# Optimization experiments

Measured on AMD Instinct MI355X. Metric: run time of the kernel, lower is better.

## Reference

```python
import jax, jax.numpy as jnp
import numpy as np

B, T_IN, N, C_IN = 4, 16, 5000, 16
HID, C_OUT, KSZ, K_CHEB = 32, 64, 3, 3
E = 80000
BN_EPS = 1e-5


def _conv1xk(x, W, b):
    # x: (B,C,N,T), W: (O,I,1,k) -> (B,O,N,T-k+1)
    y = jax.lax.conv_general_dilated(x, W, (1, 1), 'VALID',
                                     dimension_numbers=('NCHW', 'OIHW', 'NCHW'))
    return y + b[None, :, None, None]


def temporal_conv(X, W1, b1, W2, b2, W3, b3):
    # X: (B,T,N,C) -> (B,T-k+1,N,O); gated temporal conv (GLU-style)
    Xp = jnp.transpose(X, (0, 3, 2, 1))  # (B,C,N,T)
    P = _conv1xk(Xp, W1, b1)
    Q = jax.nn.sigmoid(_conv1xk(Xp, W2, b2))
    R = _conv1xk(Xp, W3, b3)
    H = jax.nn.relu(P * Q + R)
    return jnp.transpose(H, (0, 3, 2, 1))


def cheb_conv(x, edge_index, edge_weight, W, b, lambda_max=2.0):
    # x: (B,T,N,C). Batched ChebConv with sym normalization (PyG semantics).
    n = x.shape[2]
    row, col = edge_index[0], edge_index[1]
    deg = jax.ops.segment_sum(edge_weight, row, num_segments=n)
    dis = jnp.where(deg > 0, deg ** -0.5, 0.0)
    w_norm = dis[row] * edge_weight * dis[col]  # (E,)

    def lhat(z):
        # A_norm z via scatter-add over edges, batched over (B,T)
        az = jnp.zeros_like(z).at[:, :, row, :].add(
            w_norm[None, None, :, None] * z[:, :, col, :])
        # L z = z - A_norm z ; L_hat = (2/lmax) L - I
        return (2.0 / lambda_max) * (z - az) - z

    Tx0 = x
    out = jnp.einsum('btnc,cd->btnd', Tx0, W[0])
    Tx1 = lhat(Tx0)
    out = out + jnp.einsum('btnc,cd->btnd', Tx1, W[1])
    for k in range(2, W.shape[0]):
        Tx2 = 2.0 * lhat(Tx1) - Tx0
        out = out + jnp.einsum('btnc,cd->btnd', Tx2, W[k])
        Tx0, Tx1 = Tx1, Tx2
    return out + b


def batch_norm_nodes(T, gamma, beta):
    # torch: permute to (B, N, T, C), BatchNorm2d(num_nodes), permute back
    Tp = jnp.transpose(T, (0, 2, 1, 3))  # (B,N,T,C)
    mean = jnp.mean(Tp, axis=(0, 2, 3), keepdims=True)
    var = jnp.mean((Tp - mean) ** 2, axis=(0, 2, 3), keepdims=True)  # biased
    Tn = (Tp - mean) / jnp.sqrt(var + BN_EPS)
    Tn = Tn * gamma[None, :, None, None] + beta[None, :, None, None]
    return jnp.transpose(Tn, (0, 2, 1, 3))


def setup_inputs() -> dict:
    key = jax.random.key(0)
    ks = jax.random.split(key, 20)
    s = 0.05
    inp = {
        'X': jax.random.normal(ks[0], (B, T_IN, N, C_IN), jnp.float32),
        'edge_index': jax.random.randint(ks[1], (2, E), 0, N, jnp.int64
                                         if jax.config.jax_enable_x64 else jnp.int32),
        'edge_weight': jax.random.uniform(ks[2], (E,), jnp.float32),
        'tc1_w1': jax.random.normal(ks[3], (HID, C_IN, 1, KSZ)) * s,
        'tc1_b1': jnp.zeros((HID,)),
        'tc1_w2': jax.random.normal(ks[4], (HID, C_IN, 1, KSZ)) * s,
        'tc1_b2': jnp.zeros((HID,)),
        'tc1_w3': jax.random.normal(ks[5], (HID, C_IN, 1, KSZ)) * s,
        'tc1_b3': jnp.zeros((HID,)),
        'cheb_W': jax.random.normal(ks[6], (K_CHEB, HID, HID)) * s,
        'cheb_b': jnp.zeros((HID,)),
        'tc2_w1': jax.random.normal(ks[7], (C_OUT, HID, 1, KSZ)) * s,
        'tc2_b1': jnp.zeros((C_OUT,)),
        'tc2_w2': jax.random.normal(ks[8], (C_OUT, HID, 1, KSZ)) * s,
        'tc2_b2': jnp.zeros((C_OUT,)),
        'tc2_w3': jax.random.normal(ks[9], (C_OUT, HID, 1, KSZ)) * s,
        'tc2_b3': jnp.zeros((C_OUT,)),
        'bn_gamma': jnp.ones((N,)),
        'bn_beta': jnp.zeros((N,)),
    }
    return inp


def reference(X, edge_index, edge_weight,
              tc1_w1, tc1_b1, tc1_w2, tc1_b2, tc1_w3, tc1_b3,
              cheb_W, cheb_b,
              tc2_w1, tc2_b1, tc2_w2, tc2_b2, tc2_w3, tc2_b3,
              bn_gamma, bn_beta):
    T0 = temporal_conv(X, tc1_w1, tc1_b1, tc1_w2, tc1_b2, tc1_w3, tc1_b3)
    T = jax.nn.relu(cheb_conv(T0, edge_index, edge_weight, cheb_W, cheb_b))
    T = temporal_conv(T, tc2_w1, tc2_b1, tc2_w2, tc2_b2, tc2_w3, tc2_b3)
    return batch_norm_nodes(T, bn_gamma, bn_beta)
```

## Files before the change

### kernel.cpp

```cpp
#include <hip/hip_runtime.h>
#include <hip/hip_bf16.h>

#define STC_N     5000
#define STC_TIN   16
#define STC_T1    14
#define STC_T2    12
#define STC_CIN   16
#define STC_CH    32
#define STC_CO    64
#define STC_BT1   56
#define STC_BT2   48
#define STC_RT1   17500
#define STC_GBLK  1280
#define STC_GWAVE (STC_GBLK*4)
#define STC_ROWB1 1792

#define STC_OFF_DEG   0
#define STC_OFF_CNT   20000
#define STC_OFF_CUR   40000
#define STC_OFF_DIS   60000
#define STC_OFF_OFFS  80000
#define STC_OFF_WN    100032
#define STC_OFF_CCOL  420032
#define STC_OFF_CW    740032
#define STC_OFF_T0    1060096
#define STC_OFF_G1    (STC_OFF_T0 + 17920000)
#define STC_OFF_G2    (STC_OFF_G1 + 17920000)
#define STC_OFF_PK2   (STC_OFF_G2 + 17920000)
#define STC_OFF_PK1   (STC_OFF_PK2 + 36864)
#define STC_OFF_PKC   (STC_OFF_PK1 + 12288)
#define STC_WS_REQ    (STC_OFF_PKC + 6144)

typedef __hip_bfloat16 bf16;
typedef short stc_s8 __attribute__((ext_vector_type(8)));
typedef float stc_f4 __attribute__((ext_vector_type(4)));

__device__ float stc_lo16(unsigned u) { return __uint_as_float(u << 16); }
__device__ float stc_hi16(unsigned u) { return __uint_as_float(u & 0xffff0000u); }
__device__ float stc_s2f(short s) {
    return __uint_as_float(((unsigned)(unsigned short)s) << 16);
}

__device__ short stc_f2bs(float f) {
    unsigned u = __float_as_uint(f);
    u = (u + 0x7FFFu + ((u >> 16) & 1u)) >> 16;
    return (short)u;
}

__global__ void STConv_9972914061616_kernel() {}

__global__ void stc_fill(float* out, int n, float val) {
    int i = blockIdx.x * 256 + threadIdx.x;
    if (i < n) out[i] = val;
}

__global__ void stc_init(int* zp,
                         const float* w1a, const float* w1b, const float* w1c,
                         const float* w2a, const float* w2b, const float* w2c,
                         const float* chW,
                         short* pk1, short* pk2, short* pkc) {
    if (blockIdx.x < 59) {
        int i = blockIdx.x * 256 + threadIdx.x;
        if (i < 15000) zp[i] = 0;
        return;
    }
    int gid = (blockIdx.x - 59) * 256 + threadIdx.x;
    if (gid >= 54 * 64) return;
    int fi = gid >> 6;
    int lane = gid & 63;
    int j = lane & 15;
    int quad = lane >> 4;
    short f[8];
    if (fi < 36) {
        int s = fi % 3;
        int cc4 = fi / 3;
        int conv = cc4 >> 2;
        int c4 = cc4 & 3;
        const float* Wp = (conv == 0) ? w2a : ((conv == 1) ? w2b : w2c);
        int och = c4 * 16 + j;
        for (int i = 0; i < 8; ++i) {
            int cc = quad * 8 + i;
            f[i] = stc_f2bs(Wp[och * 96 + cc * 3 + s]);
        }
        for (int i = 0; i < 8; ++i) pk2[(fi * 64 + lane) * 8 + i] = f[i];
    } else if (fi < 48) {
        int t = fi - 36;
        int s = t & 1;
        int cj = t >> 1;
        int conv = cj >> 1;
        int jt = cj & 1;
        const float* Wp = (conv == 0) ? w1a : ((conv == 1) ? w1b : w1c);
        int och = jt * 16 + j;
        for (int i = 0; i < 8; ++i) {
            int k = s * 32 + quad * 8 + i;
            int kt = k >> 4;
            int c = k & 15;
            f[i] = (kt < 3) ? stc_f2bs(Wp[och * 48 + c * 3 + kt]) : (short)0;
        }
        for (int i = 0; i < 8; ++i) pk1[(t * 64 + lane) * 8 + i] = f[i];
    } else {
        int t = fi - 48;
        int s = t >> 1;
        int jt = t & 1;
        int d = jt * 16 + j;
        for (int i = 0; i < 8; ++i) {
            int c = quad * 8 + i;
            float w0 = chW[c * 32 + d];
            float w1 = chW[1024 + c * 32 + d];
            float w2 = chW[2048 + c * 32 + d];
            float v = (s == 0) ? (w0 - w2) : ((s == 1) ? -w1 : 2.0f * w2);
            f[i] = stc_f2bs(v);
        }
        for (int i = 0; i < 8; ++i) pkc[(t * 64 + lane) * 8 + i] = f[i];
    }
}

__global__ void stc_deg(const int* ei, const float* ew, float* deg, int E) {
    int e = blockIdx.x * 256 + threadIdx.x;
    if (e < E) atomicAdd(&deg[ei[e]], ew[e]);
}

__global__ void stc_wnorm(const int* ei, const float* ew, const float* deg,
                          float* wn, int* cnt, int E) {
    int e = blockIdx.x * 256 + threadIdx.x;
    if (e < E) {
        int r = ei[e];
        int c = ei[E + e];
        float dr = deg[r];
        float dc = deg[c];
        float ir = (dr > 0.0f) ? rsqrtf(dr) : 0.0f;
        float ic = (dc > 0.0f) ? rsqrtf(dc) : 0.0f;
        wn[e] = ir * ew[e] * ic;
        atomicAdd(&cnt[r], 1);
    }
}

__global__ void stc_scan(const int* cnt, int* offs, int n) {
    __shared__ int s[256];
    int tid = threadIdx.x;
    int base = tid * 20;
    int loc[20];
    int sum = 0;
#pragma unroll
    for (int k = 0; k < 20; ++k) {
        int i = base + k;
        int v = (i < n) ? cnt[i] : 0;
        loc[k] = sum;
        sum += v;
    }
    s[tid] = sum;
    __syncthreads();
    for (int off = 1; off < 256; off <<= 1) {
        int t = (tid >= off) ? s[tid - off] : 0;
        __syncthreads();
        s[tid] += t;
        __syncthreads();
    }
    int pre = (tid > 0) ? s[tid - 1] : 0;
#pragma unroll
    for (int k = 0; k < 20; ++k) {
        int i = base + k;
        if (i < n) offs[i] = pre + loc[k];
    }
    if (tid == 255) offs[n] = s[255];
}

__global__ void stc_scatter(const int* ei, const float* wn, const int* offs,
                            int* cursor, int* ccol, float* cw, int E) {
    int e = blockIdx.x * 256 + threadIdx.x;
    if (e < E) {
        int r = ei[e];
        int pos = atomicAdd(&cursor[r], 1);
        int slot = offs[r] + pos;
        ccol[slot] = ei[E + e];
        cw[slot] = wn[e];
    }
}

__global__ __launch_bounds__(256, 2) void stc_tconv1m(
    const float* X, const short* pk1,
    const float* B1, const float* B2, const float* B3,
    bf16* T0) {
    int lane = threadIdx.x & 63;
    int j = lane & 15;
    int quad = lane >> 4;
    int wave = blockIdx.x * 4 + (threadIdx.x >> 6);

    stc_s8 bfrag[3][2][2];
    for (int conv = 0; conv < 3; ++conv)
        for (int jt = 0; jt < 2; ++jt)
            for (int s = 0; s < 2; ++s) {
                int t = (conv * 2 + jt) * 2 + s;
                bfrag[conv][jt][s] = *(const stc_s8*)(pk1 + (t * 64 + lane) * 8);
            }
    float pb[2], qb[2], rb[2];
    for (int jt = 0; jt < 2; ++jt) {
        int och = jt * 16 + j;
        pb[jt] = B1[och];
        qb[jt] = B2[och];
        rb[jt] = B3[och];
    }

    for (int rt = wave; rt < STC_RT1; rt += STC_GWAVE) {
        int rm = rt * 16 + j;
        int n = rm % STC_N;
        int bt = rm / STC_N;
        int t = bt % STC_T1;
        int b = bt / STC_T1;

        int kt0 = quad >> 1;
        int c0 = (quad & 1) * 8;
        const float* xp0 = X + ((size_t)((b * STC_TIN + t + kt0) * STC_N + n)) * STC_CIN + c0;
        stc_s8 af0;
        for (int i = 0; i < 8; ++i) af0[i] = stc_f2bs(xp0[i]);

        stc_s8 af1;
        if (quad < 2) {
            const float* xp1 = X + ((size_t)((b * STC_TIN + t + 2) * STC_N + n)) * STC_CIN + c0;
            for (int i = 0; i < 8; ++i) af1[i] = stc_f2bs(xp1[i]);
        } else {
            for (int i = 0; i < 8; ++i) af1[i] = 0;
        }

        stc_f4 acc[6];
        for (int a = 0; a < 6; ++a) acc[a] = (stc_f4){0.0f, 0.0f, 0.0f, 0.0f};
        for (int conv = 0; conv < 3; ++conv) {
            for (int jt = 0; jt < 2; ++jt) {
                int a = conv * 2 + jt;
                acc[a] = __builtin_amdgcn_mfma_f32_16x16x32_bf16(
                    af0, bfrag[conv][jt][0], acc[a], 0, 0, 0);
                acc[a] = __builtin_amdgcn_mfma_f32_16x16x32_bf16(
                    af1, bfrag[conv][jt][1], acc[a], 0, 0, 0);
            }
        }

        for (int jt = 0; jt < 2; ++jt) {
            for (int reg = 0; reg < 4; ++reg) {
                float P = acc[jt][reg] + pb[jt];
                float Q = acc[2 + jt][reg] + qb[jt];
                float R = acc[4 + jt][reg] + rb[jt];
                float Qc = fminf(fmaxf(Q, -30.0f), 30.0f);
                float sg = 1.0f / (1.0f + __expf(-Qc));
                float h = P * sg + R;
                if (h < 0.0f) h = 0.0f;
                int row = rt * 16 + quad * 4 + reg;
                int nw = row % STC_N;
                int btw = row / STC_N;
                T0[(size_t)nw * STC_ROWB1 + btw * STC_CH + jt * 16 + j] =
                    __float2bfloat16(h);
            }
        }
    }
}

__global__ void stc_gatherv(const bf16* z, bf16* g, const int* offs,
                            const int* ccol, const float* cw) {
    int n = blockIdx.x;
    __shared__ int col_s[128];
    __shared__ float w_s[128];
    int beg = offs[n];
    int end = offs[n + 1];
    int cg = threadIdx.x & 3;
    int sl = threadIdx.x >> 2;
    int act = (sl < STC_BT1);
    float a0 = 0.f, a1 = 0.f, a2 = 0.f, a3 = 0.f;
    float a4 = 0.f, a5 = 0.f, a6 = 0.f, a7 = 0.f;
    const bf16* zb = z + sl * STC_CH + cg * 8;
    for (int chunk = beg; chunk < end; chunk += 128) {
        int m = end - chunk;
        if (m > 128) m = 128;
        if (threadIdx.x < m) {
            col_s[threadIdx.x] = ccol[chunk + threadIdx.x];
            w_s[threadIdx.x] = cw[chunk + threadIdx.x];
        }
        __syncthreads();
        if (act) {
            int i = 0;
            for (; i + 4 <= m; i += 4) {
                float w0 = w_s[i], w1 = w_s[i + 1], w2 = w_s[i + 2], w3 = w_s[i + 3];
                uint4 u0 = *(const uint4*)(zb + (size_t)col_s[i] * STC_ROWB1);
                uint4 u1 = *(const uint4*)(zb + (size_t)col_s[i + 1] * STC_ROWB1);
                uint4 u2 = *(const uint4*)(zb + (size_t)col_s[i + 2] * STC_ROWB1);
                uint4 u3 = *(const uint4*)(zb + (size_t)col_s[i + 3] * STC_ROWB1);
                a0 += w0 * stc_lo16(u0.x); a1 += w0 * stc_hi16(u0.x);
                a2 += w0 * stc_lo16(u0.y); a3 += w0 * stc_hi16(u0.y);
                a4 += w0 * stc_lo16(u0.z); a5 += w0 * stc_hi16(u0.z);
                a6 += w0 * stc_lo16(u0.w); a7 += w0 * stc_hi16(u0.w);
                a0 += w1 * stc_lo16(u1.x); a1 += w1 * stc_hi16(u1.x);
                a2 += w1 * stc_lo16(u1.y); a3 += w1 * stc_hi16(u1.y);
                a4 += w1 * stc_lo16(u1.z); a5 += w1 * stc_hi16(u1.z);
                a6 += w1 * stc_lo16(u1.w); a7 += w1 * stc_hi16(u1.w);
                a0 += w2 * stc_lo16(u2.x); a1 += w2 * stc_hi16(u2.x);
                a2 += w2 * stc_lo16(u2.y); a3 += w2 * stc_hi16(u2.y);
                a4 += w2 * stc_lo16(u2.z); a5 += w2 * stc_hi16(u2.z);
                a6 += w2 * stc_lo16(u2.w); a7 += w2 * stc_hi16(u2.w);
                a0 += w3 * stc_lo16(u3.x); a1 += w3 * stc_hi16(u3.x);
                a2 += w3 * stc_lo16(u3.y); a3 += w3 * stc_hi16(u3.y);
                a4 += w3 * stc_lo16(u3.z); a5 += w3 * stc_hi16(u3.z);
                a6 += w3 * stc_lo16(u3.w); a7 += w3 * stc_hi16(u3.w);
            }
            for (; i < m; ++i) {
                float w = w_s[i];
                uint4 u = *(const uint4*)(zb + (size_t)col_s[i] * STC_ROWB1);
                a0 += w * stc_lo16(u.x); a1 += w * stc_hi16(u.x);
                a2 += w * stc_lo16(u.y); a3 += w * stc_hi16(u.y);
                a4 += w * stc_lo16(u.z); a5 += w * stc_hi16(u.z);
                a6 += w * stc_lo16(u.w); a7 += w * stc_hi16(u.w);
            }
        }
        __syncthreads();
    }
    if (act) {
        unsigned p0 = ((unsigned)(unsigned short)stc_f2bs(a0)) |
                      (((unsigned)(unsigned short)stc_f2bs(a1)) << 16);
        unsigned p1 = ((unsigned)(unsigned short)stc_f2bs(a2)) |
                      (((unsigned)(unsigned short)stc_f2bs(a3)) << 16);
        unsigned p2 = ((unsigned)(unsigned short)stc_f2bs(a4)) |
                      (((unsigned)(unsigned short)stc_f2bs(a5)) << 16);
        unsigned p3 = ((unsigned)(unsigned short)stc_f2bs(a6)) |
                      (((unsigned)(unsigned short)stc_f2bs(a7)) << 16);
        uint4 o;
        o.x = p0; o.y = p1; o.z = p2; o.w = p3;
        *(uint4*)(g + (size_t)n * STC_ROWB1 + sl * STC_CH + cg * 8) = o;
    }
}

__global__ __launch_bounds__(256, 2) void stc_combconv2bn(
    const bf16* T0, const bf16* G1, const bf16* G2,
    const short* pkc, const float* chB,
    const short* pk2, const float* B1, const float* B2, const float* B3,
    const float* gamma, const float* beta, float* T2) {
    __shared__ short comb[64 * 40];
    __shared__ short hb[48 * 72];
    __shared__ float red[8];
    int lane = threadIdx.x & 63;
    int j = lane & 15;
    int quad = lane >> 4;
    int w = threadIdx.x >> 6;
    int n = blockIdx.x;

    {
        stc_s8 cfrag[3][2];
        for (int s = 0; s < 3; ++s)
            for (int jt = 0; jt < 2; ++jt)
                cfrag[s][jt] = *(const stc_s8*)(pkc + ((s * 2 + jt) * 64 + lane) * 8);
        float bl0 = chB[j];
        float bl1 = chB[16 + j];
        size_t rm = (size_t)n * STC_BT1 + w * 16 + j;
        size_t abase = rm * STC_CH + quad * 8;
        stc_s8 a0 = *(const stc_s8*)(T0 + abase);
        stc_s8 a1 = *(const stc_s8*)(G1 + abase);
        stc_s8 a2 = *(const stc_s8*)(G2 + abase);
        stc_f4 acc[2];
        acc[0] = (stc_f4){0.0f, 0.0f, 0.0f, 0.0f};
        acc[1] = (stc_f4){0.0f, 0.0f, 0.0f, 0.0f};
        for (int jt = 0; jt < 2; ++jt) {
            acc[jt] = __builtin_amdgcn_mfma_f32_16x16x32_bf16(a0, cfrag[0][jt], acc[jt], 0, 0, 0);
            acc[jt] = __builtin_amdgcn_mfma_f32_16x16x32_bf16(a1, cfrag[1][jt], acc[jt], 0, 0, 0);
            acc[jt] = __builtin_amdgcn_mfma_f32_16x16x32_bf16(a2, cfrag[2][jt], acc[jt], 0, 0, 0);
        }
        for (int jt = 0; jt < 2; ++jt) {
            float bl = (jt == 0) ? bl0 : bl1;
            for (int reg = 0; reg < 4; ++reg) {
                float h = acc[jt][reg] + bl;
                if (h < 0.0f) h = 0.0f;
                int row = w * 16 + quad * 4 + reg;
                comb[row * 40 + jt * 16 + j] = stc_f2bs(h);
            }
        }
    }
    __syncthreads();

    stc_s8 bfrag[3][3];
    for (int conv = 0; conv < 3; ++conv)
        for (int s = 0; s < 3; ++s) {
            int fi = (conv * 4 + w) * 3 + s;
            bfrag[conv][s] = *(const stc_s8*)(pk2 + (fi * 64 + lane) * 8);
        }
    int och = w * 16 + j;
    float pb = B1[och];
    float qb = B2[och];
    float rb = B3[och];

    float lsum = 0.0f;
    for (int t3 = 0; t3 < 3; ++t3) {
        int btb = t3 * 16;
        int bt2 = btb + j;
        int b = bt2 / STC_T2;
        int t = bt2 % STC_T2;
        const short* ap = comb + (b * STC_T1 + t) * 40 + quad * 8;
        stc_s8 af0 = *(const stc_s8*)(ap);
        stc_s8 af1 = *(const stc_s8*)(ap + 40);
        stc_s8 af2 = *(const stc_s8*)(ap + 80);

        stc_f4 acc[3];
        for (int a = 0; a < 3; ++a) acc[a] = (stc_f4){0.0f, 0.0f, 0.0f, 0.0f};
        for (int conv = 0; conv < 3; ++conv) {
            acc[conv] = __builtin_amdgcn_mfma_f32_16x16x32_bf16(
                af0, bfrag[conv][0], acc[conv], 0, 0, 0);
            acc[conv] = __builtin_amdgcn_mfma_f32_16x16x32_bf16(
                af1, bfrag[conv][1], acc[conv], 0, 0, 0);
            acc[conv] = __builtin_amdgcn_mfma_f32_16x16x32_bf16(
                af2, bfrag[conv][2], acc[conv], 0, 0, 0);
        }

        for (int reg = 0; reg < 4; ++reg) {
            float P = acc[0][reg] + pb;
            float Q = acc[1][reg] + qb;
            float R = acc[2][reg] + rb;
            float Qc = fminf(fmaxf(Q, -30.0f), 30.0f);
            float sg = 1.0f / (1.0f + __expf(-Qc));
            float h = P * sg + R;
            if (h < 0.0f) h = 0.0f;
            short hs = stc_f2bs(h);
            int row = btb + quad * 4 + reg;
            hb[row * 72 + w * 16 + j] = hs;
            lsum += stc_s2f(hs);
        }
    }
    for (int off = 32; off; off >>= 1) lsum += __shfl_xor(lsum, off);
    if (lane == 0) red[w] = lsum;
    __syncthreads();

    float mean = (red[0] + red[1] + red[2] + red[3]) * (1.0f / (STC_BT2 * STC_CO));

    int colc = threadIdx.x & 63;
    int rw0 = threadIdx.x >> 6;
    float sq = 0.0f;
    for (int it = 0; it < 12; ++it) {
        int row = it * 4 + rw0;
        float d = stc_s2f(hb[row * 72 + colc]) - mean;
        sq += d * d;
    }
    for (int off = 32; off; off >>= 1) sq += __shfl_xor(sq, off);
    if (lane == 0) red[4 + w] = sq;
    __syncthreads();
    float var = (red[4] + red[5] + red[6] + red[7]) * (1.0f / (STC_BT2 * STC_CO));
    float istd = rsqrtf(var + 1e-5f);
    float scale = istd * gamma[n];
    float shift = beta[n] - mean * scale;
    for (int it = 0; it < 12; ++it) {
        int row = it * 4 + rw0;
        T2[((size_t)row * STC_N + n) * STC_CO + colc] =
            stc_s2f(hb[row * 72 + colc]) * scale + shift;
    }
}

extern "C" void kernel_launch(void* const* d_in, const int* in_sizes, int n_in,
                              void* d_out, int out_size, void* d_ws, size_t ws_size,
                              hipStream_t stream) {
    float* out = (float*)d_out;
    int outb = (out_size + 255) / 256;

    if (n_in < 19) {
        stc_fill<<<outb, 256, 0, stream>>>(out, out_size, 60.0f);
        return;
    }
    if (ws_size < (size_t)STC_WS_REQ) {
        stc_fill<<<outb, 256, 0, stream>>>(out, out_size, 50.0f);
        return;
    }

    const float* X = (const float*)d_in[0];
    const int* ei = (const int*)d_in[1];
    const float* ew = (const float*)d_in[2];
    const float* w1a = (const float*)d_in[3];
    const float* b1a = (const float*)d_in[4];
    const float* w1b = (const float*)d_in[5];
    const float* b1b = (const float*)d_in[6];
    const float* w1c = (const float*)d_in[7];
    const float* b1c = (const float*)d_in[8];
    const float* chW = (const float*)d_in[9];
    const float* chB = (const float*)d_in[10];
    const float* w2a = (const float*)d_in[11];
    const float* b2a = (const float*)d_in[12];
    const float* w2b = (const float*)d_in[13];
    const float* b2b = (const float*)d_in[14];
    const float* w2c = (const float*)d_in[15];
    const float* b2c = (const float*)d_in[16];
    const float* gam = (const float*)d_in[17];
    const float* bet = (const float*)d_in[18];
    int E = in_sizes[1] / 2;

    char* ws = (char*)d_ws;
    float* deg = (float*)(ws + STC_OFF_DEG);
    int* cnt = (int*)(ws + STC_OFF_CNT);
    int* cursor = (int*)(ws + STC_OFF_CUR);
    int* offs = (int*)(ws + STC_OFF_OFFS);
    float* wn = (float*)(ws + STC_OFF_WN);
    int* ccol = (int*)(ws + STC_OFF_CCOL);
    float* cw = (float*)(ws + STC_OFF_CW);
    bf16* T0 = (bf16*)(ws + STC_OFF_T0);
    bf16* G1 = (bf16*)(ws + STC_OFF_G1);
    bf16* G2 = (bf16*)(ws + STC_OFF_G2);
    short* pk2 = (short*)(ws + STC_OFF_PK2);
    short* pk1 = (short*)(ws + STC_OFF_PK1);
    short* pkc = (short*)(ws + STC_OFF_PKC);

    stc_init<<<73, 256, 0, stream>>>((int*)(ws + STC_OFF_DEG),
                                     w1a, w1b, w1c, w2a, w2b, w2c, chW,
                                     pk1, pk2, pkc);
    stc_deg<<<(E + 255) / 256, 256, 0, stream>>>(ei, ew, deg, E);
    stc_wnorm<<<(E + 255) / 256, 256, 0, stream>>>(ei, ew, deg, wn, cnt, E);
    stc_scan<<<1, 256, 0, stream>>>(cnt, offs, STC_N);
    stc_scatter<<<(E + 255) / 256, 256, 0, stream>>>(ei, wn, offs, cursor, ccol, cw, E);
    stc_tconv1m<<<STC_GBLK, 256, 0, stream>>>(X, pk1, b1a, b1b, b1c, T0);
    stc_gatherv<<<STC_N, 256, 0, stream>>>(T0, G1, offs, ccol, cw);
    stc_gatherv<<<STC_N, 256, 0, stream>>>(G1, G2, offs, ccol, cw);
    stc_combconv2bn<<<STC_N, 256, 0, stream>>>(
        T0, G1, G2, pkc, chB, pk2, b2a, b2b, b2c, gam, bet, out);
}
```

Measured before the change: 257.0 us.

## Fuse second graph gather into combine/conv2/BN kernel and merge edge-norm kernels

```diff
diff --git a/kernel.cpp b/kernel.cpp
--- a/kernel.cpp
+++ b/kernel.cpp
@@ -115,22 +115,11 @@
     }
 }
 
-__global__ void stc_deg(const int* ei, const float* ew, float* deg, int E) {
-    int e = blockIdx.x * 256 + threadIdx.x;
-    if (e < E) atomicAdd(&deg[ei[e]], ew[e]);
-}
-
-__global__ void stc_wnorm(const int* ei, const float* ew, const float* deg,
-                          float* wn, int* cnt, int E) {
+__global__ void stc_deg(const int* ei, const float* ew, float* deg, int* cnt, int E) {
     int e = blockIdx.x * 256 + threadIdx.x;
     if (e < E) {
         int r = ei[e];
-        int c = ei[E + e];
-        float dr = deg[r];
-        float dc = deg[c];
-        float ir = (dr > 0.0f) ? rsqrtf(dr) : 0.0f;
-        float ic = (dc > 0.0f) ? rsqrtf(dc) : 0.0f;
-        wn[e] = ir * ew[e] * ic;
+        atomicAdd(&deg[r], ew[e]);
         atomicAdd(&cnt[r], 1);
     }
 }
@@ -165,15 +154,21 @@
     if (tid == 255) offs[n] = s[255];
 }
 
-__global__ void stc_scatter(const int* ei, const float* wn, const int* offs,
-                            int* cursor, int* ccol, float* cw, int E) {
+__global__ void stc_scatter(const int* ei, const float* ew, const float* deg,
+                            const int* offs, int* cursor, int* ccol, float* cw,
+                            int E) {
     int e = blockIdx.x * 256 + threadIdx.x;
     if (e < E) {
         int r = ei[e];
+        int c = ei[E + e];
+        float dr = deg[r];
+        float dc = deg[c];
+        float ir = (dr > 0.0f) ? rsqrtf(dr) : 0.0f;
+        float ic = (dc > 0.0f) ? rsqrtf(dc) : 0.0f;
         int pos = atomicAdd(&cursor[r], 1);
         int slot = offs[r] + pos;
-        ccol[slot] = ei[E + e];
-        cw[slot] = wn[e];
+        ccol[slot] = c;
+        cw[slot] = ir * ew[e] * ic;
     }
 }
 
@@ -325,19 +320,91 @@
     }
 }
 
-__global__ __launch_bounds__(256, 2) void stc_combconv2bn(
-    const bf16* T0, const bf16* G1, const bf16* G2,
+__global__ __launch_bounds__(256, 2) void stc_gcombconv2bn(
+    const bf16* T0, const bf16* G1,
+    const int* offs, const int* ccol, const float* cw,
     const short* pkc, const float* chB,
     const short* pk2, const float* B1, const float* B2, const float* B3,
     const float* gamma, const float* beta, float* T2) {
     __shared__ short comb[64 * 40];
+    __shared__ short g2[64 * 40];
     __shared__ short hb[48 * 72];
+    __shared__ int col_s[128];
+    __shared__ float w_s[128];
     __shared__ float red[8];
     int lane = threadIdx.x & 63;
     int j = lane & 15;
     int quad = lane >> 4;
     int w = threadIdx.x >> 6;
     int n = blockIdx.x;
+
+    {
+        int beg = offs[n];
+        int end = offs[n + 1];
+        int cg = threadIdx.x & 3;
+        int sl = threadIdx.x >> 2;
+        int act = (sl < STC_BT1);
+        float a0 = 0.f, a1 = 0.f, a2 = 0.f, a3 = 0.f;
+        float a4 = 0.f, a5 = 0.f, a6 = 0.f, a7 = 0.f;
+        const bf16* zb = G1 + sl * STC_CH + cg * 8;
+        for (int chunk = beg; chunk < end; chunk += 128) {
+            int m = end - chunk;
+            if (m > 128) m = 128;
+            if (threadIdx.x < m) {
+                col_s[threadIdx.x] = ccol[chunk + threadIdx.x];
+                w_s[threadIdx.x] = cw[chunk + threadIdx.x];
+            }
+            __syncthreads();
+            if (act) {
+                int i = 0;
+                for (; i + 4 <= m; i += 4) {
+                    float w0 = w_s[i], w1 = w_s[i + 1], w2 = w_s[i + 2], w3 = w_s[i + 3];
+                    uint4 u0 = *(const uint4*)(zb + (size_t)col_s[i] * STC_ROWB1);
+                    uint4 u1 = *(const uint4*)(zb + (size_t)col_s[i + 1] * STC_ROWB1);
+                    uint4 u2 = *(const uint4*)(zb + (size_t)col_s[i + 2] * STC_ROWB1);
+                    uint4 u3 = *(const uint4*)(zb + (size_t)col_s[i + 3] * STC_ROWB1);
+                    a0 += w0 * stc_lo16(u0.x); a1 += w0 * stc_hi16(u0.x);
+                    a2 += w0 * stc_lo16(u0.y); a3 += w0 * stc_hi16(u0.y);
+                    a4 += w0 * stc_lo16(u0.z); a5 += w0 * stc_hi16(u0.z);
+                    a6 += w0 * stc_lo16(u0.w); a7 += w0 * stc_hi16(u0.w);
+                    a0 += w1 * stc_lo16(u1.x); a1 += w1 * stc_hi16(u1.x);
+                    a2 += w1 * stc_lo16(u1.y); a3 += w1 * stc_hi16(u1.y);
+                    a4 += w1 * stc_lo16(u1.z); a5 += w1 * stc_hi16(u1.z);
+                    a6 += w1 * stc_lo16(u1.w); a7 += w1 * stc_hi16(u1.w);
+                    a0 += w2 * stc_lo16(u2.x); a1 += w2 * stc_hi16(u2.x);
+                    a2 += w2 * stc_lo16(u2.y); a3 += w2 * stc_hi16(u2.y);
+                    a4 += w2 * stc_lo16(u2.z); a5 += w2 * stc_hi16(u2.z);
+                    a6 += w2 * stc_lo16(u2.w); a7 += w2 * stc_hi16(u2.w);
+                    a0 += w3 * stc_lo16(u3.x); a1 += w3 * stc_hi16(u3.x);
+                    a2 += w3 * stc_lo16(u3.y); a3 += w3 * stc_hi16(u3.y);
+                    a4 += w3 * stc_lo16(u3.z); a5 += w3 * stc_hi16(u3.z);
+                    a6 += w3 * stc_lo16(u3.w); a7 += w3 * stc_hi16(u3.w);
+                }
+                for (; i < m; ++i) {
+                    float wv = w_s[i];
+                    uint4 u = *(const uint4*)(zb + (size_t)col_s[i] * STC_ROWB1);
+                    a0 += wv * stc_lo16(u.x); a1 += wv * stc_hi16(u.x);
+                    a2 += wv * stc_lo16(u.y); a3 += wv * stc_hi16(u.y);
+                    a4 += wv * stc_lo16(u.z); a5 += wv * stc_hi16(u.z);
+                    a6 += wv * stc_lo16(u.w); a7 += wv * stc_hi16(u.w);
+                }
+            }
+            __syncthreads();
+        }
+        unsigned p0 = ((unsigned)(unsigned short)stc_f2bs(a0)) |
+                      (((unsigned)(unsigned short)stc_f2bs(a1)) << 16);
+        unsigned p1 = ((unsigned)(unsigned short)stc_f2bs(a2)) |
+                      (((unsigned)(unsigned short)stc_f2bs(a3)) << 16);
+        unsigned p2 = ((unsigned)(unsigned short)stc_f2bs(a4)) |
+                      (((unsigned)(unsigned short)stc_f2bs(a5)) << 16);
+        unsigned p3 = ((unsigned)(unsigned short)stc_f2bs(a6)) |
+                      (((unsigned)(unsigned short)stc_f2bs(a7)) << 16);
+        uint4* gp = (uint4*)(g2 + sl * 40 + cg * 8);
+        uint4 o;
+        o.x = p0; o.y = p1; o.z = p2; o.w = p3;
+        *gp = o;
+    }
+    __syncthreads();
 
     {
         stc_s8 cfrag[3][2];
@@ -350,7 +417,7 @@
         size_t abase = rm * STC_CH + quad * 8;
         stc_s8 a0 = *(const stc_s8*)(T0 + abase);
         stc_s8 a1 = *(const stc_s8*)(G1 + abase);
-        stc_s8 a2 = *(const stc_s8*)(G2 + abase);
+        stc_s8 a2 = *(const stc_s8*)(g2 + (w * 16 + j) * 40 + quad * 8);
         stc_f4 acc[2];
         acc[0] = (stc_f4){0.0f, 0.0f, 0.0f, 0.0f};
         acc[1] = (stc_f4){0.0f, 0.0f, 0.0f, 0.0f};
@@ -487,12 +554,10 @@
     int* cnt = (int*)(ws + STC_OFF_CNT);
     int* cursor = (int*)(ws + STC_OFF_CUR);
     int* offs = (int*)(ws + STC_OFF_OFFS);
-    float* wn = (float*)(ws + STC_OFF_WN);
     int* ccol = (int*)(ws + STC_OFF_CCOL);
     float* cw = (float*)(ws + STC_OFF_CW);
     bf16* T0 = (bf16*)(ws + STC_OFF_T0);
     bf16* G1 = (bf16*)(ws + STC_OFF_G1);
-    bf16* G2 = (bf16*)(ws + STC_OFF_G2);
     short* pk2 = (short*)(ws + STC_OFF_PK2);
     short* pk1 = (short*)(ws + STC_OFF_PK1);
     short* pkc = (short*)(ws + STC_OFF_PKC);
@@ -500,13 +565,11 @@
     stc_init<<<73, 256, 0, stream>>>((int*)(ws + STC_OFF_DEG),
                                      w1a, w1b, w1c, w2a, w2b, w2c, chW,
                                      pk1, pk2, pkc);
-    stc_deg<<<(E + 255) / 256, 256, 0, stream>>>(ei, ew, deg, E);
-    stc_wnorm<<<(E + 255) / 256, 256, 0, stream>>>(ei, ew, deg, wn, cnt, E);
+    stc_deg<<<(E + 255) / 256, 256, 0, stream>>>(ei, ew, deg, cnt, E);
     stc_scan<<<1, 256, 0, stream>>>(cnt, offs, STC_N);
-    stc_scatter<<<(E + 255) / 256, 256, 0, stream>>>(ei, wn, offs, cursor, ccol, cw, E);
+    stc_scatter<<<(E + 255) / 256, 256, 0, stream>>>(ei, ew, deg, offs, cursor, ccol, cw, E);
     stc_tconv1m<<<STC_GBLK, 256, 0, stream>>>(X, pk1, b1a, b1b, b1c, T0);
     stc_gatherv<<<STC_N, 256, 0, stream>>>(T0, G1, offs, ccol, cw);
-    stc_gatherv<<<STC_N, 256, 0, stream>>>(G1, G2, offs, ccol, cw);
-    stc_combconv2bn<<<STC_N, 256, 0, stream>>>(
-        T0, G1, G2, pkc, chB, pk2, b2a, b2b, b2c, gam, bet, out);
-}
+    stc_gcombconv2bn<<<STC_N, 256, 0, stream>>>(
+        T0, G1, offs, ccol, cw, pkc, chB, pk2, b2a, b2b, b2c, gam, bet, out);
+}
```

New measurement: 248.2 us. 1.04x faster.
